# Performance work log

Hardware: AMD Instinct MI355X
Metric: run time of the kernel (lower is better)

## Reference

```python
import jax, jax.numpy as jnp
import numpy as np

H = 1024        # hidden_dim
MD = 2048       # memory_dim
L = 16384       # memory length == max_length
N = 8           # head_N
# sys.float_info.min underflows to 0.0 in float32, exactly as in the torch
# original (python float * float32 tensor). Kept for faithfulness.
TINY = jnp.float32(2.2250738585072014e-308)


def setup_inputs() -> dict:
    key = jax.random.key(0)
    ks = jax.random.split(key, 12)
    s_h = 1.0 / np.sqrt(H)
    s_m = 1.0 / np.sqrt(MD)
    s_o = 1.0 / np.sqrt(2 * H)
    return {
        "x": jax.random.normal(ks[0], (1, 1, H), jnp.float32),
        "memory": jax.random.normal(ks[1], (L, MD), jnp.float32),
        "Wq": jax.random.uniform(ks[2], (H, H), jnp.float32, -s_h, s_h),
        "bq": jax.random.uniform(ks[3], (H,), jnp.float32, -s_h, s_h),
        "Wk": jax.random.uniform(ks[4], (H, MD), jnp.float32, -s_m, s_m),
        "bk": jax.random.uniform(ks[5], (H,), jnp.float32, -s_m, s_m),
        "Wv": jax.random.uniform(ks[6], (H, MD), jnp.float32, -s_m, s_m),
        "bv": jax.random.uniform(ks[7], (H,), jnp.float32, -s_m, s_m),
        "Wo": jax.random.uniform(ks[8], (H, 2 * H), jnp.float32, -s_o, s_o),
        "bo": jax.random.uniform(ks[9], (H,), jnp.float32, -s_o, s_o),
    }


def reference(x, memory, Wq, bq, Wk, bk, Wv, bv, Wo, bo):
    d = H // N  # per-head dim
    # Q: (1,H) -> (1,d,N) -> (N,1,d), scaled by d**-0.5
    q = x.reshape(1, -1) @ Wq.T + bq
    Q = q.reshape(1, d, N).transpose(2, 0, 1) * (d ** -0.5)
    # K: (L,H) -> (L,d,N) -> (N,d,L)
    K = (memory @ Wk.T + bk).reshape(-1, d, N).transpose(2, 1, 0)
    QK = jnp.einsum('nod,ndl->nol', Q, K)  # (N,1,L)
    # pad mask: 1 where the memory row sums to zero, else 0 (as in torch nonzero-set)
    any_zero = memory.sum(axis=1)
    pad_mask = (any_zero == 0).astype(QK.dtype)[None, None, :]
    QK = QK + pad_mask * TINY
    attn = jax.nn.softmax(QK, axis=-1)
    # V: (L,H) -> (L,d,N) -> (N,L,d)
    V = (memory @ Wv.T + bv).reshape(-1, d, N).transpose(2, 0, 1)
    feat = jnp.einsum('nol,nld->nod', attn, V)      # (N,1,d)
    feat = feat.transpose(1, 2, 0).reshape(1, 1, H)  # (1,1,H)
    ax = jnp.concatenate([x, feat], axis=-1)         # (1,1,2H)
    return jax.nn.relu(ax @ Wo.T + bo)
```

## Files before the change

kernel.cpp:

```cpp
#include <hip/hip_runtime.h>
#include <math.h>

#define LROWS 16384
#define HDIM  1024
#define MDIM  2048
#define NH    8
#define RSQRT_D 0.08838834764831844f

#define OFF_W     0
#define OFF_BETA  16384
#define OFF_Z     16392
#define OFF_Y     16400
#define OFF_SMAX  32784
#define OFF_Q     32792
#define OFF_FEAT  33816
#define OFF_S     34840

__device__ __forceinline__ float dot4(float4 a, float4 b) {
  return a.x * b.x + a.y * b.y + a.z * b.z + a.w * b.w;
}
__device__ __forceinline__ void fma4(float4& acc, float s, float4 v) {
  acc.x = fmaf(s, v.x, acc.x); acc.y = fmaf(s, v.y, acc.y);
  acc.z = fmaf(s, v.z, acc.z); acc.w = fmaf(s, v.w, acc.w);
}

__device__ void atomicMaxF(float* addr, float v) {
  int* ai = (int*)addr;
  int old = __float_as_int(-3.4e38f);
  while (v > __int_as_float(old)) {
    int assumed = old;
    old = atomicCAS(ai, assumed, __float_as_int(v));
    if (old == assumed) break;
  }
}

__global__ __launch_bounds__(256) void k1_q(const float* __restrict__ x,
                                            const float* __restrict__ Wq,
                                            const float* __restrict__ bq,
                                            const float* __restrict__ bk,
                                            float* __restrict__ ws) {
  int tid = threadIdx.x, lane = tid & 63;
  if (blockIdx.x == 0 && tid < 8) ws[OFF_SMAX + tid] = -3.4e38f;
  int j = blockIdx.x * 4 + (tid >> 6);
  const float4* xr = (const float4*)x;
  const float4* wr = (const float4*)(Wq + (size_t)j * HDIM);
  float acc = 0.f;
#pragma unroll
  for (int i = 0; i < 4; ++i) {
    int idx = i * 64 + lane;
    acc += dot4(xr[idx], wr[idx]);
  }
#pragma unroll
  for (int off = 32; off; off >>= 1) acc += __shfl_xor(acc, off);
  if (lane == 0) {
    float qj = acc + bq[j];
    ws[OFF_Q + j] = qj;
    atomicAdd(&ws[OFF_BETA + (j & 7)], qj * bk[j]);
  }
}

__global__ __launch_bounds__(256) void k2_w(const float* __restrict__ Wk,
                                            float* __restrict__ ws) {
  int tid = threadIdx.x;
  int mc = blockIdx.x & 7, cc = blockIdx.x >> 3;
  int m = mc * 256 + tid;
  const float* q = ws + OFF_Q;
  float acc[8];
#pragma unroll
  for (int n = 0; n < 8; ++n) acc[n] = 0.f;
  int c0 = cc * 64;
  for (int c = c0; c < c0 + 64; c += 8) {
#pragma unroll
    for (int u = 0; u < 8; ++u)
      acc[u] = fmaf(q[c + u], Wk[(size_t)(c + u) * MDIM + m], acc[u]);
  }
#pragma unroll
  for (int n = 0; n < 8; ++n) atomicAdd(&ws[OFF_W + n * MDIM + m], acc[n]);
}

__global__ __launch_bounds__(256) void k3_s(const float* __restrict__ mem,
                                            float* __restrict__ ws) {
  __shared__ float sred[4 * 32 * 33];
  __shared__ float redmax[2][8];
  int tid = threadIdx.x, lane = tid & 63, wv = tid >> 6;
  int r0 = blockIdx.x * 16 + wv * 4;
  const float* wmat = ws + OFF_W;
  float acc[4][8];
#pragma unroll
  for (int rr = 0; rr < 4; ++rr)
#pragma unroll
    for (int n = 0; n < 8; ++n) acc[rr][n] = 0.f;

  for (int step = 0; step < 8; ++step) {
    int mq = step * 64 + lane;
    float4 wvv[8];
#pragma unroll
    for (int n = 0; n < 8; ++n)
      wvv[n] = *(const float4*)(wmat + n * MDIM + mq * 4);
#pragma unroll
    for (int rr = 0; rr < 4; ++rr) {
      float4 mv = *(const float4*)(mem + (size_t)(r0 + rr) * MDIM + mq * 4);
#pragma unroll
      for (int n = 0; n < 8; ++n) {
        acc[rr][n] = fmaf(mv.x, wvv[n].x, acc[rr][n]);
        acc[rr][n] = fmaf(mv.y, wvv[n].y, acc[rr][n]);
        acc[rr][n] = fmaf(mv.z, wvv[n].z, acc[rr][n]);
        acc[rr][n] = fmaf(mv.w, wvv[n].w, acc[rr][n]);
      }
    }
  }
#pragma unroll
  for (int rr = 0; rr < 4; ++rr)
#pragma unroll
    for (int n = 0; n < 8; ++n) acc[rr][n] += __shfl_xor(acc[rr][n], 32);
  if (lane < 32) {
#pragma unroll
    for (int rr = 0; rr < 4; ++rr)
#pragma unroll
      for (int n = 0; n < 8; ++n)
        sred[wv * 1056 + lane * 33 + rr * 8 + n] = acc[rr][n];
  }
  __syncthreads();

  if (tid < 128) {
    int rowl = tid >> 3, n = tid & 7;
    int wvx = rowl >> 2, rr = rowl & 3;
    const float* base = sred + wvx * 1056 + rr * 8 + n;
    float s = 0.f;
#pragma unroll
    for (int l = 0; l < 32; ++l) s += base[l * 33];
    s = (s + ws[OFF_BETA + n]) * RSQRT_D;
    int r = blockIdx.x * 16 + rowl;
    ws[OFF_S + (size_t)r * 8 + n] = s;
    float mx = s;
    mx = fmaxf(mx, __shfl_xor(mx, 8));
    mx = fmaxf(mx, __shfl_xor(mx, 16));
    mx = fmaxf(mx, __shfl_xor(mx, 32));
    if (lane < 8) redmax[tid >> 6][lane] = mx;
  }
  __syncthreads();
  if (tid < 8) atomicMaxF(&ws[OFF_SMAX + tid], fmaxf(redmax[0][tid], redmax[1][tid]));
}

__global__ __launch_bounds__(256) void k5_y(const float* __restrict__ mem,
                                            float* __restrict__ ws) {
  __shared__ float pLds[256 * 8];
  __shared__ float4 sred[4 * 8 * 32];
  int tid = threadIdx.x;
  int cb = blockIdx.x & 15, rc = blockIdx.x >> 4;
  int r0 = rc * 256;
  {
    const float4* srow = (const float4*)(ws + OFF_S + (size_t)(r0 + tid) * 8);
    float4 mx0 = *(const float4*)(ws + OFF_SMAX);
    float4 mx1 = *(const float4*)(ws + OFF_SMAX + 4);
    float4 s0 = srow[0], s1 = srow[1];
    float4 e0, e1;
    e0.x = __expf(s0.x - mx0.x); e0.y = __expf(s0.y - mx0.y);
    e0.z = __expf(s0.z - mx0.z); e0.w = __expf(s0.w - mx0.w);
    e1.x = __expf(s1.x - mx1.x); e1.y = __expf(s1.y - mx1.y);
    e1.z = __expf(s1.z - mx1.z); e1.w = __expf(s1.w - mx1.w);
    ((float4*)pLds)[tid * 2] = e0;
    ((float4*)pLds)[tid * 2 + 1] = e1;
    if (cb == 0) {
      float v0x = e0.x, v0y = e0.y, v0z = e0.z, v0w = e0.w;
      float v1x = e1.x, v1y = e1.y, v1z = e1.z, v1w = e1.w;
#pragma unroll
      for (int off = 32; off; off >>= 1) {
        v0x += __shfl_xor(v0x, off); v0y += __shfl_xor(v0y, off);
        v0z += __shfl_xor(v0z, off); v0w += __shfl_xor(v0w, off);
        v1x += __shfl_xor(v1x, off); v1y += __shfl_xor(v1y, off);
        v1z += __shfl_xor(v1z, off); v1w += __shfl_xor(v1w, off);
      }
      if ((tid & 63) == 0) {
        atomicAdd(&ws[OFF_Z + 0], v0x); atomicAdd(&ws[OFF_Z + 1], v0y);
        atomicAdd(&ws[OFF_Z + 2], v0z); atomicAdd(&ws[OFF_Z + 3], v0w);
        atomicAdd(&ws[OFF_Z + 4], v1x); atomicAdd(&ws[OFF_Z + 5], v1y);
        atomicAdd(&ws[OFF_Z + 6], v1z); atomicAdd(&ws[OFF_Z + 7], v1w);
      }
    }
  }
  __syncthreads();
  int mq = cb * 32 + (tid & 31);
  int ro = tid >> 5;
  float4 acc[8];
#pragma unroll
  for (int n = 0; n < 8; ++n) acc[n] = make_float4(0.f, 0.f, 0.f, 0.f);
  for (int i = 0; i < 32; ++i) {
    int rl = i * 8 + ro;
    float4 mv = *(const float4*)(mem + (size_t)(r0 + rl) * MDIM + mq * 4);
    float4 p0 = ((const float4*)pLds)[rl * 2];
    float4 p1 = ((const float4*)pLds)[rl * 2 + 1];
    fma4(acc[0], p0.x, mv); fma4(acc[1], p0.y, mv);
    fma4(acc[2], p0.z, mv); fma4(acc[3], p0.w, mv);
    fma4(acc[4], p1.x, mv); fma4(acc[5], p1.y, mv);
    fma4(acc[6], p1.z, mv); fma4(acc[7], p1.w, mv);
  }
  int lane = tid & 63, w = tid >> 6;
#pragma unroll
  for (int n = 0; n < 8; ++n) {
    acc[n].x += __shfl_xor(acc[n].x, 32); acc[n].y += __shfl_xor(acc[n].y, 32);
    acc[n].z += __shfl_xor(acc[n].z, 32); acc[n].w += __shfl_xor(acc[n].w, 32);
  }
  if (lane < 32) {
#pragma unroll
    for (int n = 0; n < 8; ++n) sred[(w * 8 + n) * 32 + lane] = acc[n];
  }
  __syncthreads();
  {
    int n = tid >> 5, ml = tid & 31;
    float4 s = sred[n * 32 + ml];
#pragma unroll
    for (int w2 = 1; w2 < 4; ++w2) {
      float4 v = sred[(w2 * 8 + n) * 32 + ml];
      s.x += v.x; s.y += v.y; s.z += v.z; s.w += v.w;
    }
    float* yb = ws + OFF_Y + n * MDIM + cb * 128 + ml * 4;
    atomicAdd(yb + 0, s.x); atomicAdd(yb + 1, s.y);
    atomicAdd(yb + 2, s.z); atomicAdd(yb + 3, s.w);
  }
}

__global__ __launch_bounds__(256) void k6_feat(const float* __restrict__ Wv,
                                               const float* __restrict__ bv,
                                               float* __restrict__ ws) {
  int tid = threadIdx.x, lane = tid & 63;
  int c = blockIdx.x * 4 + (tid >> 6);
  int n = c & 7;
  const float4* yb = (const float4*)(ws + OFF_Y + n * MDIM);
  const float4* wb = (const float4*)(Wv + (size_t)c * MDIM);
  float acc = 0.f;
#pragma unroll
  for (int s = 0; s < 8; ++s) {
    int idx = s * 64 + lane;
    acc += dot4(yb[idx], wb[idx]);
  }
#pragma unroll
  for (int off = 32; off; off >>= 1) acc += __shfl_xor(acc, off);
  if (lane == 0) ws[OFF_FEAT + c] = acc / ws[OFF_Z + n] + bv[c];
}

__global__ __launch_bounds__(256) void k7_out(const float* __restrict__ x,
                                              const float* __restrict__ Wo,
                                              const float* __restrict__ bo,
                                              const float* __restrict__ ws,
                                              float* __restrict__ out) {
  int tid = threadIdx.x, lane = tid & 63;
  int j = blockIdx.x * 4 + (tid >> 6);
  const float4* wb = (const float4*)(Wo + (size_t)j * 2048);
  const float4* xr = (const float4*)x;
  const float4* fr = (const float4*)(ws + OFF_FEAT);
  float acc = 0.f;
#pragma unroll
  for (int s = 0; s < 4; ++s) {
    int idx = s * 64 + lane;
    acc += dot4(xr[idx], wb[idx]);
    acc += dot4(fr[idx], wb[256 + idx]);
  }
#pragma unroll
  for (int off = 32; off; off >>= 1) acc += __shfl_xor(acc, off);
  if (lane == 0) out[j] = fmaxf(acc + bo[j], 0.f);
}

extern "C" void kernel_launch(void* const* d_in, const int* in_sizes, int n_in,
                              void* d_out, int out_size, void* d_ws, size_t ws_size,
                              hipStream_t stream) {
  const float* x   = (const float*)d_in[0];
  const float* mem = (const float*)d_in[1];
  const float* Wq  = (const float*)d_in[2];
  const float* bq  = (const float*)d_in[3];
  const float* Wk  = (const float*)d_in[4];
  const float* bk  = (const float*)d_in[5];
  const float* Wv  = (const float*)d_in[6];
  const float* bv  = (const float*)d_in[7];
  const float* Wo  = (const float*)d_in[8];
  const float* bo  = (const float*)d_in[9];
  float* ws  = (float*)d_ws;
  float* out = (float*)d_out;

  hipMemsetAsync(ws, 0, OFF_SMAX * sizeof(float), stream);

  k1_q   <<<256,  256, 0, stream>>>(x, Wq, bq, bk, ws);
  k2_w   <<<128,  256, 0, stream>>>(Wk, ws);
  k3_s   <<<1024, 256, 0, stream>>>(mem, ws);
  k5_y   <<<1024, 256, 0, stream>>>(mem, ws);
  k6_feat<<<256,  256, 0, stream>>>(Wv, bv, ws);
  k7_out <<<256,  256, 0, stream>>>(x, Wo, bo, ws, out);
}
```

Baseline: 310.6 us.

## Fuse score and weighted-sum passes over memory, drop max pass and atomics

Merges the score kernel and the value-accumulation kernel into one, so each block computes scores for its 32 rows and then immediately accumulates exp(score)-weighted memory rows while they are likely still cached. This avoids a second full read of the large memory matrix and a round trip of the score buffer. The global max reduction is dropped and exp is applied to raw scores, which is exact algebra but risks overflow on inputs with large scores. Per-block partial results now go to a large workspace buffer and are summed by a new reduction kernel instead of global float atomics, which adds extra write and read traffic.

```diff
diff --git a/kernel.cpp b/kernel.cpp
--- a/kernel.cpp
+++ b/kernel.cpp
@@ -10,11 +10,10 @@
 #define OFF_W     0
 #define OFF_BETA  16384
 #define OFF_Z     16392
-#define OFF_Y     16400
-#define OFF_SMAX  32784
-#define OFF_Q     32792
-#define OFF_FEAT  33816
-#define OFF_S     34840
+#define OFF_Q     16400
+#define OFF_FEAT  17424
+#define OFF_Y     18448
+#define OFF_YBUF  34832
 
 __device__ __forceinline__ float dot4(float4 a, float4 b) {
   return a.x * b.x + a.y * b.y + a.z * b.z + a.w * b.w;
@@ -23,15 +22,8 @@
   acc.x = fmaf(s, v.x, acc.x); acc.y = fmaf(s, v.y, acc.y);
   acc.z = fmaf(s, v.z, acc.z); acc.w = fmaf(s, v.w, acc.w);
 }
-
-__device__ void atomicMaxF(float* addr, float v) {
-  int* ai = (int*)addr;
-  int old = __float_as_int(-3.4e38f);
-  while (v > __int_as_float(old)) {
-    int assumed = old;
-    old = atomicCAS(ai, assumed, __float_as_int(v));
-    if (old == assumed) break;
-  }
+__device__ __forceinline__ void add4(float4& a, float4 v) {
+  a.x += v.x; a.y += v.y; a.z += v.z; a.w += v.w;
 }
 
 __global__ __launch_bounds__(256) void k1_q(const float* __restrict__ x,
@@ -40,7 +32,6 @@
                                             const float* __restrict__ bk,
                                             float* __restrict__ ws) {
   int tid = threadIdx.x, lane = tid & 63;
-  if (blockIdx.x == 0 && tid < 8) ws[OFF_SMAX + tid] = -3.4e38f;
   int j = blockIdx.x * 4 + (tid >> 6);
   const float4* xr = (const float4*)x;
   const float4* wr = (const float4*)(Wq + (size_t)j * HDIM);
@@ -78,145 +69,119 @@
   for (int n = 0; n < 8; ++n) atomicAdd(&ws[OFF_W + n * MDIM + m], acc[n]);
 }
 
-__global__ __launch_bounds__(256) void k3_s(const float* __restrict__ mem,
-                                            float* __restrict__ ws) {
+__global__ __launch_bounds__(256, 2) void k35(const float* __restrict__ mem,
+                                              float* __restrict__ ws) {
   __shared__ float sred[4 * 32 * 33];
-  __shared__ float redmax[2][8];
+  __shared__ float4 pv4[32];
   int tid = threadIdx.x, lane = tid & 63, wv = tid >> 6;
-  int r0 = blockIdx.x * 16 + wv * 4;
   const float* wmat = ws + OFF_W;
-  float acc[4][8];
-#pragma unroll
-  for (int rr = 0; rr < 4; ++rr)
-#pragma unroll
-    for (int n = 0; n < 8; ++n) acc[rr][n] = 0.f;
-
-  for (int step = 0; step < 8; ++step) {
-    int mq = step * 64 + lane;
-    float4 wvv[8];
-#pragma unroll
-    for (int n = 0; n < 8; ++n)
-      wvv[n] = *(const float4*)(wmat + n * MDIM + mq * 4);
-#pragma unroll
-    for (int rr = 0; rr < 4; ++rr) {
-      float4 mv = *(const float4*)(mem + (size_t)(r0 + rr) * MDIM + mq * 4);
-#pragma unroll
-      for (int n = 0; n < 8; ++n) {
-        acc[rr][n] = fmaf(mv.x, wvv[n].x, acc[rr][n]);
-        acc[rr][n] = fmaf(mv.y, wvv[n].y, acc[rr][n]);
-        acc[rr][n] = fmaf(mv.z, wvv[n].z, acc[rr][n]);
-        acc[rr][n] = fmaf(mv.w, wvv[n].w, acc[rr][n]);
+  float* pv = (float*)pv4;
+
+  float4 y0[8], y1[8];
+#pragma unroll
+  for (int n = 0; n < 8; ++n) {
+    y0[n] = make_float4(0.f, 0.f, 0.f, 0.f);
+    y1[n] = make_float4(0.f, 0.f, 0.f, 0.f);
+  }
+  float zacc = 0.f;
+
+  for (int g = 0; g < 2; ++g) {
+    int r0 = blockIdx.x * 32 + g * 16;
+    float acc[4][8];
+#pragma unroll
+    for (int rr = 0; rr < 4; ++rr)
+#pragma unroll
+      for (int n = 0; n < 8; ++n) acc[rr][n] = 0.f;
+    for (int step = 0; step < 8; ++step) {
+      int mq = step * 64 + lane;
+      float4 wvv[8];
+#pragma unroll
+      for (int n = 0; n < 8; ++n)
+        wvv[n] = *(const float4*)(wmat + n * MDIM + mq * 4);
+#pragma unroll
+      for (int rr = 0; rr < 4; ++rr) {
+        float4 mv = *(const float4*)(mem + (size_t)(r0 + wv * 4 + rr) * MDIM + mq * 4);
+#pragma unroll
+        for (int n = 0; n < 8; ++n) {
+          acc[rr][n] = fmaf(mv.x, wvv[n].x, acc[rr][n]);
+          acc[rr][n] = fmaf(mv.y, wvv[n].y, acc[rr][n]);
+          acc[rr][n] = fmaf(mv.z, wvv[n].z, acc[rr][n]);
+          acc[rr][n] = fmaf(mv.w, wvv[n].w, acc[rr][n]);
+        }
       }
     }
-  }
-#pragma unroll
-  for (int rr = 0; rr < 4; ++rr)
-#pragma unroll
-    for (int n = 0; n < 8; ++n) acc[rr][n] += __shfl_xor(acc[rr][n], 32);
-  if (lane < 32) {
 #pragma unroll
     for (int rr = 0; rr < 4; ++rr)
 #pragma unroll
-      for (int n = 0; n < 8; ++n)
-        sred[wv * 1056 + lane * 33 + rr * 8 + n] = acc[rr][n];
-  }
+      for (int n = 0; n < 8; ++n) acc[rr][n] += __shfl_xor(acc[rr][n], 32);
+    if (lane < 32) {
+#pragma unroll
+      for (int rr = 0; rr < 4; ++rr)
+#pragma unroll
+        for (int n = 0; n < 8; ++n)
+          sred[wv * 1056 + lane * 33 + rr * 8 + n] = acc[rr][n];
+    }
+    __syncthreads();
+    if (tid < 128) {
+      int rowl = tid >> 3, n = tid & 7;
+      int wvx = rowl >> 2, rr = rowl & 3;
+      const float* base = sred + wvx * 1056 + rr * 8 + n;
+      float s = 0.f;
+#pragma unroll
+      for (int l = 0; l < 32; ++l) s += base[l * 33];
+      s = (s + ws[OFF_BETA + n]) * RSQRT_D;
+      float p = __expf(s);
+      pv[rowl * 8 + n] = p;
+      zacc += p;
+    }
+    __syncthreads();
+#pragma unroll 4
+    for (int rl = 0; rl < 16; ++rl) {
+      const float* row = mem + (size_t)(r0 + rl) * MDIM;
+      float4 m0 = *(const float4*)(row + tid * 4);
+      float4 m1 = *(const float4*)(row + 1024 + tid * 4);
+      float4 pA = pv4[rl * 2];
+      float4 pB = pv4[rl * 2 + 1];
+      fma4(y0[0], pA.x, m0); fma4(y1[0], pA.x, m1);
+      fma4(y0[1], pA.y, m0); fma4(y1[1], pA.y, m1);
+      fma4(y0[2], pA.z, m0); fma4(y1[2], pA.z, m1);
+      fma4(y0[3], pA.w, m0); fma4(y1[3], pA.w, m1);
+      fma4(y0[4], pB.x, m0); fma4(y1[4], pB.x, m1);
+      fma4(y0[5], pB.y, m0); fma4(y1[5], pB.y, m1);
+      fma4(y0[6], pB.z, m0); fma4(y1[6], pB.z, m1);
+      fma4(y0[7], pB.w, m0); fma4(y1[7], pB.w, m1);
+    }
+    __syncthreads();
+  }
+  float* yb = ws + OFF_YBUF + (size_t)blockIdx.x * 16384;
+#pragma unroll
+  for (int n = 0; n < 8; ++n) {
+    *(float4*)(yb + n * MDIM + tid * 4) = y0[n];
+    *(float4*)(yb + n * MDIM + 1024 + tid * 4) = y1[n];
+  }
+  if (tid < 128) {
+    float z = zacc;
+    z += __shfl_xor(z, 8); z += __shfl_xor(z, 16); z += __shfl_xor(z, 32);
+    if ((tid & 63) < 8) atomicAdd(&ws[OFF_Z + (tid & 7)], z);
+  }
+}
+
+__global__ __launch_bounds__(256) void k4c(float* __restrict__ ws) {
+  __shared__ float4 sA[256];
+  int t = threadIdx.x;
+  int quad = blockIdx.x * 16 + (t & 15);
+  int b0 = (t >> 4) * 32;
+  const float4* src = (const float4*)(ws + OFF_YBUF);
+  float4 acc = make_float4(0.f, 0.f, 0.f, 0.f);
+  for (int b = b0; b < b0 + 32; ++b)
+    add4(acc, src[(size_t)b * 4096 + quad]);
+  sA[(t & 15) * 16 + (t >> 4)] = acc;
   __syncthreads();
-
-  if (tid < 128) {
-    int rowl = tid >> 3, n = tid & 7;
-    int wvx = rowl >> 2, rr = rowl & 3;
-    const float* base = sred + wvx * 1056 + rr * 8 + n;
-    float s = 0.f;
-#pragma unroll
-    for (int l = 0; l < 32; ++l) s += base[l * 33];
-    s = (s + ws[OFF_BETA + n]) * RSQRT_D;
-    int r = blockIdx.x * 16 + rowl;
-    ws[OFF_S + (size_t)r * 8 + n] = s;
-    float mx = s;
-    mx = fmaxf(mx, __shfl_xor(mx, 8));
-    mx = fmaxf(mx, __shfl_xor(mx, 16));
-    mx = fmaxf(mx, __shfl_xor(mx, 32));
-    if (lane < 8) redmax[tid >> 6][lane] = mx;
-  }
-  __syncthreads();
-  if (tid < 8) atomicMaxF(&ws[OFF_SMAX + tid], fmaxf(redmax[0][tid], redmax[1][tid]));
-}
-
-__global__ __launch_bounds__(256) void k5_y(const float* __restrict__ mem,
-                                            float* __restrict__ ws) {
-  __shared__ float pLds[256 * 8];
-  __shared__ float4 sred[4 * 8 * 32];
-  int tid = threadIdx.x;
-  int cb = blockIdx.x & 15, rc = blockIdx.x >> 4;
-  int r0 = rc * 256;
-  {
-    const float4* srow = (const float4*)(ws + OFF_S + (size_t)(r0 + tid) * 8);
-    float4 mx0 = *(const float4*)(ws + OFF_SMAX);
-    float4 mx1 = *(const float4*)(ws + OFF_SMAX + 4);
-    float4 s0 = srow[0], s1 = srow[1];
-    float4 e0, e1;
-    e0.x = __expf(s0.x - mx0.x); e0.y = __expf(s0.y - mx0.y);
-    e0.z = __expf(s0.z - mx0.z); e0.w = __expf(s0.w - mx0.w);
-    e1.x = __expf(s1.x - mx1.x); e1.y = __expf(s1.y - mx1.y);
-    e1.z = __expf(s1.z - mx1.z); e1.w = __expf(s1.w - mx1.w);
-    ((float4*)pLds)[tid * 2] = e0;
-    ((float4*)pLds)[tid * 2 + 1] = e1;
-    if (cb == 0) {
-      float v0x = e0.x, v0y = e0.y, v0z = e0.z, v0w = e0.w;
-      float v1x = e1.x, v1y = e1.y, v1z = e1.z, v1w = e1.w;
-#pragma unroll
-      for (int off = 32; off; off >>= 1) {
-        v0x += __shfl_xor(v0x, off); v0y += __shfl_xor(v0y, off);
-        v0z += __shfl_xor(v0z, off); v0w += __shfl_xor(v0w, off);
-        v1x += __shfl_xor(v1x, off); v1y += __shfl_xor(v1y, off);
-        v1z += __shfl_xor(v1z, off); v1w += __shfl_xor(v1w, off);
-      }
-      if ((tid & 63) == 0) {
-        atomicAdd(&ws[OFF_Z + 0], v0x); atomicAdd(&ws[OFF_Z + 1], v0y);
-        atomicAdd(&ws[OFF_Z + 2], v0z); atomicAdd(&ws[OFF_Z + 3], v0w);
-        atomicAdd(&ws[OFF_Z + 4], v1x); atomicAdd(&ws[OFF_Z + 5], v1y);
-        atomicAdd(&ws[OFF_Z + 6], v1z); atomicAdd(&ws[OFF_Z + 7], v1w);
-      }
-    }
-  }
-  __syncthreads();
-  int mq = cb * 32 + (tid & 31);
-  int ro = tid >> 5;
-  float4 acc[8];
-#pragma unroll
-  for (int n = 0; n < 8; ++n) acc[n] = make_float4(0.f, 0.f, 0.f, 0.f);
-  for (int i = 0; i < 32; ++i) {
-    int rl = i * 8 + ro;
-    float4 mv = *(const float4*)(mem + (size_t)(r0 + rl) * MDIM + mq * 4);
-    float4 p0 = ((const float4*)pLds)[rl * 2];
-    float4 p1 = ((const float4*)pLds)[rl * 2 + 1];
-    fma4(acc[0], p0.x, mv); fma4(acc[1], p0.y, mv);
-    fma4(acc[2], p0.z, mv); fma4(acc[3], p0.w, mv);
-    fma4(acc[4], p1.x, mv); fma4(acc[5], p1.y, mv);
-    fma4(acc[6], p1.z, mv); fma4(acc[7], p1.w, mv);
-  }
-  int lane = tid & 63, w = tid >> 6;
-#pragma unroll
-  for (int n = 0; n < 8; ++n) {
-    acc[n].x += __shfl_xor(acc[n].x, 32); acc[n].y += __shfl_xor(acc[n].y, 32);
-    acc[n].z += __shfl_xor(acc[n].z, 32); acc[n].w += __shfl_xor(acc[n].w, 32);
-  }
-  if (lane < 32) {
-#pragma unroll
-    for (int n = 0; n < 8; ++n) sred[(w * 8 + n) * 32 + lane] = acc[n];
-  }
-  __syncthreads();
-  {
-    int n = tid >> 5, ml = tid & 31;
-    float4 s = sred[n * 32 + ml];
-#pragma unroll
-    for (int w2 = 1; w2 < 4; ++w2) {
-      float4 v = sred[(w2 * 8 + n) * 32 + ml];
-      s.x += v.x; s.y += v.y; s.z += v.z; s.w += v.w;
-    }
-    float* yb = ws + OFF_Y + n * MDIM + cb * 128 + ml * 4;
-    atomicAdd(yb + 0, s.x); atomicAdd(yb + 1, s.y);
-    atomicAdd(yb + 2, s.z); atomicAdd(yb + 3, s.w);
+  if (t < 16) {
+    float4 s = sA[t * 16];
+#pragma unroll
+    for (int j = 1; j < 16; ++j) add4(s, sA[t * 16 + j]);
+    ((float4*)(ws + OFF_Y))[blockIdx.x * 16 + t] = s;
   }
 }
 
@@ -277,12 +242,12 @@
   float* ws  = (float*)d_ws;
   float* out = (float*)d_out;
 
-  hipMemsetAsync(ws, 0, OFF_SMAX * sizeof(float), stream);
-
-  k1_q   <<<256,  256, 0, stream>>>(x, Wq, bq, bk, ws);
-  k2_w   <<<128,  256, 0, stream>>>(Wk, ws);
-  k3_s   <<<1024, 256, 0, stream>>>(mem, ws);
-  k5_y   <<<1024, 256, 0, stream>>>(mem, ws);
-  k6_feat<<<256,  256, 0, stream>>>(Wv, bv, ws);
-  k7_out <<<256,  256, 0, stream>>>(x, Wo, bo, ws, out);
-}
+  hipMemsetAsync(ws, 0, OFF_Q * sizeof(float), stream);
+
+  k1_q   <<<256, 256, 0, stream>>>(x, Wq, bq, bk, ws);
+  k2_w   <<<128, 256, 0, stream>>>(Wk, ws);
+  k35    <<<512, 256, 0, stream>>>(mem, ws);
+  k4c    <<<256, 256, 0, stream>>>(ws);
+  k6_feat<<<256, 256, 0, stream>>>(Wv, bv, ws);
+  k7_out <<<256, 256, 0, stream>>>(x, Wo, bo, ws, out);
+}
```

Result: faster. 300.7 us (-3.2%).
